# Performance work log

Hardware: AMD Instinct MI355X
Metric: run time of the kernel (lower is better)

The kernel has to match this reference:

```python
import jax, jax.numpy as jnp
import numpy as np

N_QUBITS = 4
N_LAYERS = 2


def _apply_1q(state, U, w):
    """Apply a single-qubit gate on wire w. state: [B]+[2]*n complex.
    U: [2,2] (shared) or [B,2,2] (per-sample)."""
    s = jnp.moveaxis(state, w + 1, -1)
    if U.ndim == 3:
        s = jnp.einsum('bij,b...j->b...i', U, s)
    else:
        s = jnp.einsum('ij,b...j->b...i', U, s)
    return jnp.moveaxis(s, -1, w + 1)


def _cnot(state, c, t):
    """CNOT with control wire c, target wire t on state [B]+[2]*n."""
    s0 = jnp.take(state, jnp.array([0]), axis=c + 1)
    s1 = jnp.take(state, jnp.array([1]), axis=c + 1)
    s1 = jnp.flip(s1, axis=t + 1)  # X on target when control=1
    return jnp.concatenate([s0, s1], axis=c + 1)


def _rot_matrix(phi, theta, omega):
    """PennyLane Rot(phi,theta,omega) = RZ(omega) RY(theta) RZ(phi)."""
    c = jnp.cos(theta / 2)
    s = jnp.sin(theta / 2)
    ep = jnp.exp(-0.5j * (phi + omega))
    em = jnp.exp(-0.5j * (phi - omega))
    row0 = jnp.stack([ep * c, -jnp.conj(em) * s])
    row1 = jnp.stack([em * s, jnp.conj(ep) * c])
    return jnp.stack([row0, row1]).astype(jnp.complex64)  # [2,2]


def _circuit(x, weights):
    n, L = N_QUBITS, N_LAYERS
    B = x.shape[0]
    angles = jnp.tanh(x[:, :n]) * jnp.float32(np.pi)  # [B, n]
    # |0...0> state, shape [B, 2,2,2,2]
    state = jnp.zeros((B,) + (2,) * n, dtype=jnp.complex64)
    state = state.at[(slice(None),) + (0,) * n].set(1.0)
    # angle encoding: RY(x_i * pi), batched gate per qubit
    for w in range(n):
        th = angles[:, w]
        c = jnp.cos(th / 2)
        s = jnp.sin(th / 2)
        U = jnp.stack([jnp.stack([c, -s], -1),
                       jnp.stack([s, c], -1)], -2).astype(jnp.complex64)  # [B,2,2]
        state = _apply_1q(state, U, w)
    # variational layers
    for l in range(L):
        for w in range(n):
            U = _rot_matrix(weights[l, w, 0], weights[l, w, 1], weights[l, w, 2])
            state = _apply_1q(state, U, w)
        for w in range(n):
            state = _cnot(state, w, (w + 1) % n)
    # <Z_i> for each wire
    probs = state.real ** 2 + state.imag ** 2  # [B]+[2]*n
    outs = []
    for w in range(n):
        p = jnp.moveaxis(probs, w + 1, 1).reshape(B, 2, -1).sum(-1)  # [B,2]
        outs.append(p[:, 0] - p[:, 1])
    return jnp.stack(outs, -1).astype(jnp.float32)  # [B, n]


def setup_inputs() -> dict:
    key = jax.random.key(0)
    k1, k2 = jax.random.split(key)
    x = jax.random.normal(k1, (524288, 8), dtype=jnp.float32)
    weights = jax.random.normal(k2, (N_LAYERS, N_QUBITS, 3), dtype=jnp.float32) * 0.1
    return {"x": x, "weights": weights}


def reference(x, weights):
    return _circuit(x, weights)
```

## Files before the change

### kernel.cpp

```cpp
#include <hip/hip_runtime.h>

#define NQ 4
#define NL 2
#define NGATES (NL * NQ)

__global__ void prep_gates(const float* __restrict__ w, float* __restrict__ g) {
    int t = threadIdx.x;
    if (t >= NGATES) return;
    float phi   = w[t * 3 + 0];
    float theta = w[t * 3 + 1];
    float omega = w[t * 3 + 2];
    float st, ct, sa, ca, sb, cb;
    sincosf(theta * 0.5f, &st, &ct);
    sincosf((phi + omega) * 0.5f, &sa, &ca);
    sincosf((phi - omega) * 0.5f, &sb, &cb);
    float* o = g + t * 8;
    o[0] = ca * ct;  o[1] = -sa * ct;
    o[2] = -cb * st; o[3] = -sb * st;
    o[4] = cb * st;  o[5] = -sb * st;
    o[6] = ca * ct;  o[7] = sa * ct;
}

__global__ __launch_bounds__(256) void qsim(const float* __restrict__ x,
                                            const float* __restrict__ g,
                                            float* __restrict__ out, int B) {
    int i = blockIdx.x * blockDim.x + threadIdx.x;
    if (i >= B) return;

    float4 xv = *reinterpret_cast<const float4*>(x + (size_t)i * 8);

    const float HALF_PI = 1.57079632679489662f;
    float cw[NQ], sw[NQ];
    {
        float a;
        a = tanhf(xv.x) * HALF_PI; __sincosf(a, &sw[0], &cw[0]);
        a = tanhf(xv.y) * HALF_PI; __sincosf(a, &sw[1], &cw[1]);
        a = tanhf(xv.z) * HALF_PI; __sincosf(a, &sw[2], &cw[2]);
        a = tanhf(xv.w) * HALF_PI; __sincosf(a, &sw[3], &cw[3]);
    }

    float sr[16], si[16];
#pragma unroll
    for (int k = 0; k < 16; ++k) {
        float v = ((k & 8) ? sw[0] : cw[0]) *
                  ((k & 4) ? sw[1] : cw[1]) *
                  ((k & 2) ? sw[2] : cw[2]) *
                  ((k & 1) ? sw[3] : cw[3]);
        sr[k] = v;
        si[k] = 0.0f;
    }

#pragma unroll
    for (int l = 0; l < NL; ++l) {
#pragma unroll
        for (int w = 0; w < NQ; ++w) {
            const float* u = g + (l * NQ + w) * 8;
            float u00r = u[0], u00i = u[1], u01r = u[2], u01i = u[3];
            float u10r = u[4], u10i = u[5], u11r = u[6], u11i = u[7];
            int st = 8 >> w;
#pragma unroll
            for (int k = 0; k < 16; ++k) {
                if (k & st) continue;
                int k1 = k + st;
                float ar = sr[k],  ai = si[k];
                float br = sr[k1], bi = si[k1];
                sr[k]  = u00r * ar - u00i * ai + u01r * br - u01i * bi;
                si[k]  = u00r * ai + u00i * ar + u01r * bi + u01i * br;
                sr[k1] = u10r * ar - u10i * ai + u11r * br - u11i * bi;
                si[k1] = u10r * ai + u10i * ar + u11r * bi + u11i * br;
            }
        }
#pragma unroll
        for (int c = 0; c < NQ; ++c) {
            int t  = (c + 1) & 3;
            int cs = 8 >> c;
            int ts = 8 >> t;
#pragma unroll
            for (int k = 0; k < 16; ++k) {
                if ((k & cs) && !(k & ts)) {
                    int k1 = k | ts;
                    float tr = sr[k]; sr[k] = sr[k1]; sr[k1] = tr;
                    float ti = si[k]; si[k] = si[k1]; si[k1] = ti;
                }
            }
        }
    }

    float p[16];
#pragma unroll
    for (int k = 0; k < 16; ++k) p[k] = sr[k] * sr[k] + si[k] * si[k];

    float4 o = {0.f, 0.f, 0.f, 0.f};
#pragma unroll
    for (int k = 0; k < 16; ++k) {
        o.x += (k & 8) ? -p[k] : p[k];
        o.y += (k & 4) ? -p[k] : p[k];
        o.z += (k & 2) ? -p[k] : p[k];
        o.w += (k & 1) ? -p[k] : p[k];
    }
    *reinterpret_cast<float4*>(out + (size_t)i * 4) = o;
}

extern "C" void kernel_launch(void* const* d_in, const int* in_sizes, int n_in,
                              void* d_out, int out_size, void* d_ws, size_t ws_size,
                              hipStream_t stream) {
    const float* x   = (const float*)d_in[0];
    const float* wts = (const float*)d_in[1];
    float* out       = (float*)d_out;
    float* gates     = (float*)d_ws;

    int B = in_sizes[0] / 8;

    prep_gates<<<1, 64, 0, stream>>>(wts, gates);

    int threads = 256;
    int blocks  = (B + threads - 1) / threads;
    qsim<<<blocks, threads, 0, stream>>>(x, gates, out, B);
}
```

Before: 85.69 us.

## Precompute full 16x16 circuit unitary and apply as real-vector matvec

Collapses all variational Rot gates and CNOTs into one 16x16 complex unitary, built once per launch by a small prep kernel that evolves each basis vector. Because the encoded state is real, the main kernel applies it as 512 FMAs against uniform gate loads, replacing the gate-by-gate complex updates. It also swaps tanhf for an exp/reciprocal approximation. The costs are 512 floats of gate data read per thread through the cache and slightly different rounding.

```diff
diff --git a/kernel.cpp b/kernel.cpp
--- a/kernel.cpp
+++ b/kernel.cpp
@@ -2,23 +2,65 @@
 
 #define NQ 4
 #define NL 2
-#define NGATES (NL * NQ)
 
-__global__ void prep_gates(const float* __restrict__ w, float* __restrict__ g) {
-    int t = threadIdx.x;
-    if (t >= NGATES) return;
-    float phi   = w[t * 3 + 0];
-    float theta = w[t * 3 + 1];
-    float omega = w[t * 3 + 2];
-    float st, ct, sa, ca, sb, cb;
-    sincosf(theta * 0.5f, &st, &ct);
-    sincosf((phi + omega) * 0.5f, &sa, &ca);
-    sincosf((phi - omega) * 0.5f, &sb, &cb);
-    float* o = g + t * 8;
-    o[0] = ca * ct;  o[1] = -sa * ct;
-    o[2] = -cb * st; o[3] = -sb * st;
-    o[4] = cb * st;  o[5] = -sb * st;
-    o[6] = ca * ct;  o[7] = sa * ct;
+__global__ void prep_unitary(const float* __restrict__ w, float* __restrict__ g) {
+    int k = threadIdx.x;
+    if (k >= 16) return;
+
+    float sr[16], si[16];
+#pragma unroll
+    for (int j = 0; j < 16; ++j) { sr[j] = 0.f; si[j] = 0.f; }
+    sr[k] = 1.f;
+
+#pragma unroll
+    for (int l = 0; l < NL; ++l) {
+#pragma unroll
+        for (int wi = 0; wi < NQ; ++wi) {
+            float phi = w[(l * NQ + wi) * 3 + 0];
+            float th  = w[(l * NQ + wi) * 3 + 1];
+            float om  = w[(l * NQ + wi) * 3 + 2];
+            float st, ct, sa, ca, sb, cb;
+            sincosf(th * 0.5f, &st, &ct);
+            sincosf((phi + om) * 0.5f, &sa, &ca);
+            sincosf((phi - om) * 0.5f, &sb, &cb);
+            float u00r =  ca * ct, u00i = -sa * ct;
+            float u01r = -cb * st, u01i = -sb * st;
+            float u10r =  cb * st, u10i = -sb * st;
+            float u11r =  ca * ct, u11i =  sa * ct;
+            int stb = 8 >> wi;
+#pragma unroll
+            for (int a = 0; a < 16; ++a) {
+                if (a & stb) continue;
+                int b = a + stb;
+                float ar = sr[a], ai = si[a], br = sr[b], bi = si[b];
+                sr[a] = u00r * ar - u00i * ai + u01r * br - u01i * bi;
+                si[a] = u00r * ai + u00i * ar + u01r * bi + u01i * br;
+                sr[b] = u10r * ar - u10i * ai + u11r * br - u11i * bi;
+                si[b] = u10r * ai + u10i * ar + u11r * bi + u11i * br;
+            }
+        }
+#pragma unroll
+        for (int c = 0; c < NQ; ++c) {
+            int t = (c + 1) & 3, cs = 8 >> c, ts = 8 >> t;
+#pragma unroll
+            for (int a = 0; a < 16; ++a) {
+                if ((a & cs) && !(a & ts)) {
+                    int b = a | ts;
+                    float tr = sr[a]; sr[a] = sr[b]; sr[b] = tr;
+                    float ti = si[a]; si[a] = si[b]; si[b] = ti;
+                }
+            }
+        }
+    }
+
+    float* o = g + k * 32;
+#pragma unroll
+    for (int j = 0; j < 16; ++j) { o[2 * j] = sr[j]; o[2 * j + 1] = si[j]; }
+}
+
+__device__ __forceinline__ float fast_tanh(float v) {
+    float e = __expf(2.0f * v);
+    return 1.0f - 2.0f * __frcp_rn(1.0f + e);
 }
 
 __global__ __launch_bounds__(256) void qsim(const float* __restrict__ x,
@@ -30,65 +72,46 @@
     float4 xv = *reinterpret_cast<const float4*>(x + (size_t)i * 8);
 
     const float HALF_PI = 1.57079632679489662f;
-    float cw[NQ], sw[NQ];
+    float c[NQ], s[NQ];
     {
         float a;
-        a = tanhf(xv.x) * HALF_PI; __sincosf(a, &sw[0], &cw[0]);
-        a = tanhf(xv.y) * HALF_PI; __sincosf(a, &sw[1], &cw[1]);
-        a = tanhf(xv.z) * HALF_PI; __sincosf(a, &sw[2], &cw[2]);
-        a = tanhf(xv.w) * HALF_PI; __sincosf(a, &sw[3], &cw[3]);
+        a = fast_tanh(xv.x) * HALF_PI; __sincosf(a, &s[0], &c[0]);
+        a = fast_tanh(xv.y) * HALF_PI; __sincosf(a, &s[1], &c[1]);
+        a = fast_tanh(xv.z) * HALF_PI; __sincosf(a, &s[2], &c[2]);
+        a = fast_tanh(xv.w) * HALF_PI; __sincosf(a, &s[3], &c[3]);
     }
 
-    float sr[16], si[16];
+    float A[4], Bq[4], s0[16];
+#pragma unroll
+    for (int a = 0; a < 4; ++a)
+        A[a] = ((a & 2) ? s[0] : c[0]) * ((a & 1) ? s[1] : c[1]);
+#pragma unroll
+    for (int b = 0; b < 4; ++b)
+        Bq[b] = ((b & 2) ? s[2] : c[2]) * ((b & 1) ? s[3] : c[3]);
+#pragma unroll
+    for (int k = 0; k < 16; ++k) s0[k] = A[k >> 2] * Bq[k & 3];
+
+    float2 psi[16];
+#pragma unroll
+    for (int j = 0; j < 16; ++j) psi[j] = make_float2(0.f, 0.f);
+
+    const float2* G = reinterpret_cast<const float2*>(g);
 #pragma unroll
     for (int k = 0; k < 16; ++k) {
-        float v = ((k & 8) ? sw[0] : cw[0]) *
-                  ((k & 4) ? sw[1] : cw[1]) *
-                  ((k & 2) ? sw[2] : cw[2]) *
-                  ((k & 1) ? sw[3] : cw[3]);
-        sr[k] = v;
-        si[k] = 0.0f;
-    }
-
+        float a = s0[k];
+        const float2* col = G + k * 16;
 #pragma unroll
-    for (int l = 0; l < NL; ++l) {
-#pragma unroll
-        for (int w = 0; w < NQ; ++w) {
-            const float* u = g + (l * NQ + w) * 8;
-            float u00r = u[0], u00i = u[1], u01r = u[2], u01i = u[3];
-            float u10r = u[4], u10i = u[5], u11r = u[6], u11i = u[7];
-            int st = 8 >> w;
-#pragma unroll
-            for (int k = 0; k < 16; ++k) {
-                if (k & st) continue;
-                int k1 = k + st;
-                float ar = sr[k],  ai = si[k];
-                float br = sr[k1], bi = si[k1];
-                sr[k]  = u00r * ar - u00i * ai + u01r * br - u01i * bi;
-                si[k]  = u00r * ai + u00i * ar + u01r * bi + u01i * br;
-                sr[k1] = u10r * ar - u10i * ai + u11r * br - u11i * bi;
-                si[k1] = u10r * ai + u10i * ar + u11r * bi + u11i * br;
-            }
-        }
-#pragma unroll
-        for (int c = 0; c < NQ; ++c) {
-            int t  = (c + 1) & 3;
-            int cs = 8 >> c;
-            int ts = 8 >> t;
-#pragma unroll
-            for (int k = 0; k < 16; ++k) {
-                if ((k & cs) && !(k & ts)) {
-                    int k1 = k | ts;
-                    float tr = sr[k]; sr[k] = sr[k1]; sr[k1] = tr;
-                    float ti = si[k]; si[k] = si[k1]; si[k1] = ti;
-                }
-            }
+        for (int j = 0; j < 16; ++j) {
+            float2 u = col[j];
+            psi[j].x = fmaf(a, u.x, psi[j].x);
+            psi[j].y = fmaf(a, u.y, psi[j].y);
         }
     }
 
     float p[16];
 #pragma unroll
-    for (int k = 0; k < 16; ++k) p[k] = sr[k] * sr[k] + si[k] * si[k];
+    for (int j = 0; j < 16; ++j)
+        p[j] = psi[j].x * psi[j].x + psi[j].y * psi[j].y;
 
     float4 o = {0.f, 0.f, 0.f, 0.f};
 #pragma unroll
@@ -111,7 +134,7 @@
 
     int B = in_sizes[0] / 8;
 
-    prep_gates<<<1, 64, 0, stream>>>(wts, gates);
+    prep_unitary<<<1, 64, 0, stream>>>(wts, gates);
 
     int threads = 256;
     int blocks  = (B + threads - 1) / threads;
```

After: 77.76 us. -9.3%, faster.
